# Kernel optimization log

Hardware: AMD Instinct MI355X
Metric: run time of the kernel (lower is better)

## Reference

```python
import jax, jax.numpy as jnp
import numpy as np

N_SEL = 8192      # total nodes across selected subgraphs
SUB_SZ = 32       # nodes per subgraph
N_SUB = 256       # number of subgraphs (N_SEL / SUB_SZ)
N_GRAPH = 64      # source graphs (4 subgraphs each)
N_FULL = 12288    # nodes in the full graph
E_RAW = 262144    # raw edges
N_PERS = 4        # weighted-cosine perspectives
D = 128           # feature dim
EPSILON = 0.1
LAMB1 = 0.5


def setup_inputs() -> dict:
    key = jax.random.key(0)
    k1, k2, k3, k4, k5 = jax.random.split(key, 5)
    x = jax.random.normal(k1, (N_SEL, D), dtype=jnp.float32)
    Wc = jax.random.normal(k2, (N_PERS, D), dtype=jnp.float32)
    selected_score = jax.random.uniform(k3, (N_SUB,), dtype=jnp.float32) + 0.1
    selected_batch = jnp.asarray(np.arange(N_SEL) // SUB_SZ, dtype=jnp.int32)
    selected_belong = jnp.asarray(np.arange(N_SUB) // (N_SUB // N_GRAPH), dtype=jnp.int32)
    # injective mapping from selected nodes -> full-graph node ids
    selected_mapping = jax.random.permutation(k4, N_FULL)[:N_SEL].astype(jnp.int32)
    # block-diagonal complete edge set within each subgraph (torch.meshgrid in prepare_parsed_data)
    base = (np.arange(N_SUB) * SUB_SZ)[:, None, None]
    r = np.broadcast_to(np.arange(SUB_SZ)[None, :, None], (N_SUB, SUB_SZ, SUB_SZ)) + base
    c = np.broadcast_to(np.arange(SUB_SZ)[None, None, :], (N_SUB, SUB_SZ, SUB_SZ)) + base
    full_edge_index = jnp.asarray(np.stack([r.ravel(), c.ravel()]), dtype=jnp.int32)
    raw_edge_index = jax.random.randint(k5, (2, E_RAW), 0, N_FULL, dtype=jnp.int32)
    return {"x": x, "Wc": Wc, "selected_score": selected_score,
            "selected_batch": selected_batch, "selected_mapping": selected_mapping,
            "selected_belong": selected_belong, "full_edge_index": full_edge_index,
            "raw_edge_index": raw_edge_index}


def reference(x, Wc, selected_score, selected_batch, selected_mapping,
              selected_belong, full_edge_index, raw_edge_index):
    # ---- per-graph scatter-normalization of subgraph scores ----
    score_sum = jax.ops.segment_sum(selected_score, selected_belong, num_segments=N_GRAPH)
    score = selected_score / score_sum[selected_belong]          # [N_SUB]

    # ---- WeightedCosine metric: dense pairwise adjacency over all selected nodes ----
    h = x[None, :, :] * Wc[:, None, :]                            # [P, N_sel, D]
    hn = h / jnp.clip(jnp.linalg.norm(h, axis=-1, keepdims=True), 1e-12)
    adj = jnp.einsum('pid,pjd->ij', hn, hn) / N_PERS              # [N_sel, N_sel]

    # ---- mask to intra-subgraph candidate edges ----
    mask = jnp.zeros((N_SEL, N_SEL), dtype=adj.dtype).at[full_edge_index[0], full_edge_index[1]].set(1.0)
    adj = adj * mask
    # EpsilonNN
    adj = adj * (adj > EPSILON).astype(adj.dtype)
    # RemoveSelfLoop
    adj = adj * (1.0 - jnp.eye(N_SEL, dtype=adj.dtype))
    # dense_to_sparse + weighting: weight each edge by its row-node's subgraph score
    attr = adj * (score[selected_batch] * LAMB1)[:, None]         # [N_sel, N_sel]

    # ---- map to full-graph ids and coalesce (duplicate-sum) into dense adjacency ----
    out = jnp.zeros((N_FULL, N_FULL), dtype=x.dtype)
    out = out.at[selected_mapping[:, None], selected_mapping[None, :]].add(attr)
    out = out.at[raw_edge_index[0], raw_edge_index[1]].add(1.0 - LAMB1)
    return out
```

## Files before the change

### kernel.cpp

```cpp
#include <hip/hip_runtime.h>

#define N_SEL 8192
#define SUB_SZ 32
#define N_SUB 256
#define N_GRAPH 64
#define N_FULL 12288
#define E_RAW 262144
#define N_PERS 4
#define D 128
#define EPSILON 0.1f
#define LAMB1 0.5f

#define CAP_E 96
#define OVF_CAP 8192

typedef float f4_t __attribute__((ext_vector_type(4)));

#define OFF_COUNTS   0
#define OFF_INVMAP   ((size_t)N_FULL * 4)
#define OFF_ATTR     (OFF_INVMAP + (size_t)N_FULL * 4)
#define OFF_RAWCOLS  (OFF_ATTR + (size_t)N_SEL * SUB_SZ * 4)
#define OFF_OVFCNT   (OFF_RAWCOLS + (size_t)N_FULL * CAP_E * 4)
#define OFF_OVF      (OFF_OVFCNT + 16)
#define WS_NEEDED    (OFF_OVF + (size_t)OVF_CAP * 8)

__global__ __launch_bounds__(256) void prep_kernel(int* __restrict__ counts,
                                                   int* __restrict__ inv_map,
                                                   int* __restrict__ ovf_cnt)
{
    int t = blockIdx.x * 256 + threadIdx.x;
    if (t < N_FULL) { counts[t] = 0; inv_map[t] = -1; }
    if (t == 0) *ovf_cnt = 0;
}

__global__ __launch_bounds__(256) void build_kernel(
        const float* __restrict__ x,
        const float* __restrict__ Wc,
        const float* __restrict__ sscore,
        const int*   __restrict__ smap,
        const int*   __restrict__ rei,
        int*   __restrict__ counts,
        int*   __restrict__ inv_map,
        float* __restrict__ attr_vals,
        int*   __restrict__ raw_cols,
        int*   __restrict__ ovf_cnt,
        uint2* __restrict__ ovf)
{
    const int tid = threadIdx.x;

    if (blockIdx.x >= N_SUB) {
        int e = (blockIdx.x - N_SUB) * 256 + tid;
        int r = rei[e];
        int c = rei[E_RAW + e];
        int slot = atomicAdd(&counts[r], 1);
        if (slot < CAP_E) {
            raw_cols[(size_t)r * CAP_E + slot] = c;
        } else {
            int o = atomicAdd(ovf_cnt, 1);
            if (o < OVF_CAP) ovf[o] = make_uint2((unsigned)r, (unsigned)c);
        }
        return;
    }

    const int s    = blockIdx.x;
    const int base = s * SUB_SZ;

    __shared__ float xs[SUB_SZ][D + 1];
    __shared__ float w2[N_PERS][D];
    __shared__ float rnorm[N_PERS][SUB_SZ];
    __shared__ float rowscore;

    for (int k = tid; k < SUB_SZ * D; k += 256) {
        int i = k >> 7;
        int d = k & (D - 1);
        xs[i][d] = x[(base + i) * D + d];
    }
    for (int k = tid; k < N_PERS * D; k += 256) {
        float w = Wc[k];
        ((float*)w2)[k] = w * w;
    }
    if (tid < SUB_SZ) inv_map[smap[base + tid]] = base + tid;
    if (tid == 0) {
        int g4 = (s >> 2) << 2;
        float sum = sscore[g4] + sscore[g4 + 1] + sscore[g4 + 2] + sscore[g4 + 3];
        rowscore = (sscore[s] / sum) * LAMB1;
    }
    __syncthreads();

    if (tid < N_PERS * SUB_SZ) {
        int p = tid >> 5;
        int i = tid & 31;
        float acc = 0.f;
        #pragma unroll 8
        for (int d = 0; d < D; ++d) {
            float v = xs[i][d];
            acc = fmaf(v * v, w2[p][d], acc);
        }
        rnorm[p][i] = 1.0f / fmaxf(sqrtf(acc), 1e-12f);
    }
    __syncthreads();

    for (int e = tid; e < SUB_SZ * SUB_SZ; e += 256) {
        int i = e >> 5;
        int j = e & 31;
        float v = 0.f;
        if (i != j) {
            float a0 = 0.f, a1 = 0.f, a2 = 0.f, a3 = 0.f;
            #pragma unroll 8
            for (int d = 0; d < D; ++d) {
                float prod = xs[i][d] * xs[j][d];
                a0 = fmaf(prod, w2[0][d], a0);
                a1 = fmaf(prod, w2[1][d], a1);
                a2 = fmaf(prod, w2[2][d], a2);
                a3 = fmaf(prod, w2[3][d], a3);
            }
            float adj = 0.25f * (a0 * rnorm[0][i] * rnorm[0][j] +
                                 a1 * rnorm[1][i] * rnorm[1][j] +
                                 a2 * rnorm[2][i] * rnorm[2][j] +
                                 a3 * rnorm[3][i] * rnorm[3][j]);
            if (adj > EPSILON) v = adj * rowscore;
        }
        attr_vals[(size_t)base * SUB_SZ + e] = v;
    }
}

__global__ __launch_bounds__(256) void rowfill_kernel(
        const int*   __restrict__ counts,
        const int*   __restrict__ inv_map,
        const float* __restrict__ attr_vals,
        const int*   __restrict__ raw_cols,
        const int*   __restrict__ smap,
        float* __restrict__ out)
{
    __shared__ float row[N_FULL];
    const int r   = blockIdx.x;
    const int tid = threadIdx.x;

    f4_t* row4 = (f4_t*)row;
    const f4_t z = (f4_t){0.f, 0.f, 0.f, 0.f};
    #pragma unroll
    for (int k = 0; k < N_FULL / 4 / 256; ++k)
        row4[tid + k * 256] = z;
    __syncthreads();

    int i = inv_map[r];
    if (i >= 0 && tid < SUB_SZ) {
        float v = attr_vals[(size_t)i * SUB_SZ + tid];
        if (v != 0.f) {
            int c = smap[(i >> 5) * SUB_SZ + tid];
            atomicAdd(&row[c], v);
        }
    }
    int cnt = counts[r];
    if (cnt > CAP_E) cnt = CAP_E;
    for (int e = tid; e < cnt; e += 256) {
        int c = raw_cols[(size_t)r * CAP_E + e];
        atomicAdd(&row[c], 1.0f - LAMB1);
    }
    __syncthreads();

    f4_t* dst = (f4_t*)(out + (size_t)r * N_FULL);
    #pragma unroll
    for (int k = 0; k < N_FULL / 4 / 256; ++k)
        __builtin_nontemporal_store(row4[tid + k * 256], &dst[tid + k * 256]);
}

__global__ __launch_bounds__(256) void ovf_kernel(const int* __restrict__ ovf_cnt,
                                                  const uint2* __restrict__ ovf,
                                                  float* __restrict__ out)
{
    int n = *ovf_cnt;
    if (n > OVF_CAP) n = OVF_CAP;
    for (int t = blockIdx.x * 256 + threadIdx.x; t < n; t += gridDim.x * 256) {
        uint2 e = ovf[t];
        atomicAdd(&out[(size_t)e.x * N_FULL + e.y], 1.0f - LAMB1);
    }
}

#define N4_TOTAL 37748736
#define FILL_BLOCKS 4096
#define PER_BLOCK (N4_TOTAL / FILL_BLOCKS)
#define FILL_ITERS (PER_BLOCK / 256)

__global__ __launch_bounds__(256) void zero_kernel(f4_t* __restrict__ out)
{
    size_t base = (size_t)blockIdx.x * PER_BLOCK + threadIdx.x;
    const f4_t z = (f4_t){0.f, 0.f, 0.f, 0.f};
    #pragma unroll
    for (int k = 0; k < FILL_ITERS; ++k)
        __builtin_nontemporal_store(z, &out[base + (size_t)k * 256]);
}

__global__ __launch_bounds__(256) void scatter_kernel(
        const float* __restrict__ x,
        const float* __restrict__ Wc,
        const float* __restrict__ sscore,
        const int*   __restrict__ smap,
        const int*   __restrict__ rei,
        float* __restrict__ out)
{
    const int tid = threadIdx.x;

    if (blockIdx.x >= N_SUB) {
        int e = (blockIdx.x - N_SUB) * 256 + tid;
        long long r = rei[e];
        long long c = rei[E_RAW + e];
        atomicAdd(&out[r * (long long)N_FULL + c], 1.0f - LAMB1);
        return;
    }

    const int s    = blockIdx.x;
    const int base = s * SUB_SZ;

    __shared__ float xs[SUB_SZ][D + 1];
    __shared__ float w2[N_PERS][D];
    __shared__ float rnorm[N_PERS][SUB_SZ];
    __shared__ int   map_s[SUB_SZ];
    __shared__ float rowscore;

    for (int k = tid; k < SUB_SZ * D; k += 256) {
        int i = k >> 7;
        int d = k & (D - 1);
        xs[i][d] = x[(base + i) * D + d];
    }
    for (int k = tid; k < N_PERS * D; k += 256) {
        float w = Wc[k];
        ((float*)w2)[k] = w * w;
    }
    if (tid < SUB_SZ) map_s[tid] = smap[base + tid];
    if (tid == 0) {
        int g4 = (s >> 2) << 2;
        float sum = sscore[g4] + sscore[g4 + 1] + sscore[g4 + 2] + sscore[g4 + 3];
        rowscore = (sscore[s] / sum) * LAMB1;
    }
    __syncthreads();

    if (tid < N_PERS * SUB_SZ) {
        int p = tid >> 5;
        int i = tid & 31;
        float acc = 0.f;
        #pragma unroll 8
        for (int d = 0; d < D; ++d) {
            float v = xs[i][d];
            acc = fmaf(v * v, w2[p][d], acc);
        }
        rnorm[p][i] = 1.0f / fmaxf(sqrtf(acc), 1e-12f);
    }
    __syncthreads();

    for (int e = tid; e < SUB_SZ * SUB_SZ; e += 256) {
        int i = e >> 5;
        int j = e & 31;
        if (i == j) continue;
        float a0 = 0.f, a1 = 0.f, a2 = 0.f, a3 = 0.f;
        #pragma unroll 8
        for (int d = 0; d < D; ++d) {
            float prod = xs[i][d] * xs[j][d];
            a0 = fmaf(prod, w2[0][d], a0);
            a1 = fmaf(prod, w2[1][d], a1);
            a2 = fmaf(prod, w2[2][d], a2);
            a3 = fmaf(prod, w2[3][d], a3);
        }
        float adj = 0.25f * (a0 * rnorm[0][i] * rnorm[0][j] +
                             a1 * rnorm[1][i] * rnorm[1][j] +
                             a2 * rnorm[2][i] * rnorm[2][j] +
                             a3 * rnorm[3][i] * rnorm[3][j]);
        if (adj > EPSILON) {
            long long row = map_s[i];
            long long col = map_s[j];
            atomicAdd(&out[row * (long long)N_FULL + col], adj * rowscore);
        }
    }
}

extern "C" void kernel_launch(void* const* d_in, const int* in_sizes, int n_in,
                              void* d_out, int out_size, void* d_ws, size_t ws_size,
                              hipStream_t stream) {
    const float* x      = (const float*)d_in[0];
    const float* Wc     = (const float*)d_in[1];
    const float* sscore = (const float*)d_in[2];
    const int* smap = (const int*)d_in[4];
    const int* rei  = (const int*)d_in[7];
    float* out = (float*)d_out;

    if (ws_size >= WS_NEEDED) {
        char* ws = (char*)d_ws;
        int*   counts    = (int*)(ws + OFF_COUNTS);
        int*   inv_map   = (int*)(ws + OFF_INVMAP);
        float* attr_vals = (float*)(ws + OFF_ATTR);
        int*   raw_cols  = (int*)(ws + OFF_RAWCOLS);
        int*   ovf_cnt   = (int*)(ws + OFF_OVFCNT);
        uint2* ovf       = (uint2*)(ws + OFF_OVF);

        prep_kernel<<<(N_FULL + 255) / 256, 256, 0, stream>>>(counts, inv_map, ovf_cnt);
        build_kernel<<<N_SUB + E_RAW / 256, 256, 0, stream>>>(
            x, Wc, sscore, smap, rei, counts, inv_map, attr_vals, raw_cols, ovf_cnt, ovf);
        rowfill_kernel<<<N_FULL, 256, 0, stream>>>(
            counts, inv_map, attr_vals, raw_cols, smap, out);
        ovf_kernel<<<16, 256, 0, stream>>>(ovf_cnt, ovf, out);
    } else {
        zero_kernel<<<FILL_BLOCKS, 256, 0, stream>>>((f4_t*)out);
        scatter_kernel<<<N_SUB + E_RAW / 256, 256, 0, stream>>>(
            x, Wc, sscore, smap, rei, out);
    }
}
```

Measured before the change: 160.4 us.

## Build dense output rows in registers instead of a 48KB shared-memory row

The row-fill kernel no longer zeroes a 48KB shared-memory row and scatters into it with atomics. It stages the up to 128 sparse (column, value) entries for the row in a small shared buffer. Each thread then scans all entries and adds the ones that fall in its own 12 float4 slots, accumulating in registers before streaming the row out. This removes the large LDS footprint that limited occupancy on a store-bandwidth-bound kernel. In exchange every thread does a serial scan of all entries, with a select chain per entry.

```diff
diff --git a/kernel.cpp b/kernel.cpp
--- a/kernel.cpp
+++ b/kernel.cpp
@@ -13,6 +13,7 @@
 
 #define CAP_E 96
 #define OVF_CAP 8192
+#define KROW 12
 
 typedef float f4_t __attribute__((ext_vector_type(4)));
 
@@ -132,37 +133,55 @@
         const int*   __restrict__ smap,
         float* __restrict__ out)
 {
-    __shared__ float row[N_FULL];
+    __shared__ uint2 ents[CAP_E + SUB_SZ];
     const int r   = blockIdx.x;
     const int tid = threadIdx.x;
 
-    f4_t* row4 = (f4_t*)row;
-    const f4_t z = (f4_t){0.f, 0.f, 0.f, 0.f};
-    #pragma unroll
-    for (int k = 0; k < N_FULL / 4 / 256; ++k)
-        row4[tid + k * 256] = z;
-    __syncthreads();
-
-    int i = inv_map[r];
-    if (i >= 0 && tid < SUB_SZ) {
-        float v = attr_vals[(size_t)i * SUB_SZ + tid];
-        if (v != 0.f) {
-            int c = smap[(i >> 5) * SUB_SZ + tid];
-            atomicAdd(&row[c], v);
-        }
-    }
     int cnt = counts[r];
     if (cnt > CAP_E) cnt = CAP_E;
-    for (int e = tid; e < cnt; e += 256) {
-        int c = raw_cols[(size_t)r * CAP_E + e];
-        atomicAdd(&row[c], 1.0f - LAMB1);
-    }
-    __syncthreads();
+    if (tid < cnt)
+        ents[tid] = make_uint2((unsigned)raw_cols[(size_t)r * CAP_E + tid],
+                               __float_as_uint(1.0f - LAMB1));
+    int i = inv_map[r];
+    int n_ent = cnt;
+    if (i >= 0) {
+        if (tid < SUB_SZ) {
+            float v = attr_vals[(size_t)i * SUB_SZ + tid];
+            int   c = smap[(i >> 5) * SUB_SZ + tid];
+            ents[cnt + tid] = make_uint2((unsigned)c, __float_as_uint(v));
+        }
+        n_ent += SUB_SZ;
+    }
+    __syncthreads();
+
+    f4_t acc[KROW];
+    #pragma unroll
+    for (int k = 0; k < KROW; ++k)
+        acc[k] = (f4_t){0.f, 0.f, 0.f, 0.f};
+
+    for (int e = 0; e < n_ent; ++e) {
+        uint2 en = ents[e];
+        unsigned c = en.x;
+        if (((c >> 2) & 255u) == (unsigned)tid) {
+            float v = __uint_as_float(en.y);
+            int k = (int)(c >> 10);
+            int j = (int)(c & 3u);
+            #pragma unroll
+            for (int kk = 0; kk < KROW; ++kk) {
+                if (kk == k) {
+                    acc[kk].x += (j == 0) ? v : 0.f;
+                    acc[kk].y += (j == 1) ? v : 0.f;
+                    acc[kk].z += (j == 2) ? v : 0.f;
+                    acc[kk].w += (j == 3) ? v : 0.f;
+                }
+            }
+        }
+    }
 
     f4_t* dst = (f4_t*)(out + (size_t)r * N_FULL);
     #pragma unroll
-    for (int k = 0; k < N_FULL / 4 / 256; ++k)
-        __builtin_nontemporal_store(row4[tid + k * 256], &dst[tid + k * 256]);
+    for (int k = 0; k < KROW; ++k)
+        __builtin_nontemporal_store(acc[k], &dst[k * 256 + tid]);
 }
 
 __global__ __launch_bounds__(256) void ovf_kernel(const int* __restrict__ ovf_cnt,
```

After: 170.4 us. 6.3% more time.

## Replace per-row LDS assembly with bitmap-guided zero fill plus sparse line patches

Applied to the files above, without the earlier changes.

Builds a bitmap of 64-byte output lines that receive nonzero entries, set by atomics during the build kernel. A single launch then has one set of blocks write zeros only to lines not in the bitmap, while per-row blocks assemble and store only the touched 16-float lines. This removes the per-row 48KB shared-memory zeroing, LDS atomics and full-row copy-out, which limited occupancy. In exchange it adds global atomicOr traffic, a bitmap read for every output vector, and a quadratic leader scan over each row's entries.

```diff
diff --git a/kernel.cpp b/kernel.cpp
--- a/kernel.cpp
+++ b/kernel.cpp
@@ -13,6 +13,8 @@
 
 #define CAP_E 96
 #define OVF_CAP 8192
+#define LPR (N_FULL / 16)
+#define BM_WORDS (N_FULL * LPR / 32)
 
 typedef float f4_t __attribute__((ext_vector_type(4)));
 
@@ -22,13 +24,16 @@
 #define OFF_RAWCOLS  (OFF_ATTR + (size_t)N_SEL * SUB_SZ * 4)
 #define OFF_OVFCNT   (OFF_RAWCOLS + (size_t)N_FULL * CAP_E * 4)
 #define OFF_OVF      (OFF_OVFCNT + 16)
-#define WS_NEEDED    (OFF_OVF + (size_t)OVF_CAP * 8)
+#define OFF_BITMAP   (OFF_OVF + (size_t)OVF_CAP * 8)
+#define WS_NEEDED    (OFF_BITMAP + (size_t)BM_WORDS * 4)
 
 __global__ __launch_bounds__(256) void prep_kernel(int* __restrict__ counts,
                                                    int* __restrict__ inv_map,
-                                                   int* __restrict__ ovf_cnt)
+                                                   int* __restrict__ ovf_cnt,
+                                                   unsigned* __restrict__ bitmap)
 {
     int t = blockIdx.x * 256 + threadIdx.x;
+    if (t < BM_WORDS) bitmap[t] = 0u;
     if (t < N_FULL) { counts[t] = 0; inv_map[t] = -1; }
     if (t == 0) *ovf_cnt = 0;
 }
@@ -44,7 +49,8 @@
         float* __restrict__ attr_vals,
         int*   __restrict__ raw_cols,
         int*   __restrict__ ovf_cnt,
-        uint2* __restrict__ ovf)
+        uint2* __restrict__ ovf,
+        unsigned* __restrict__ bitmap)
 {
     const int tid = threadIdx.x;
 
@@ -55,6 +61,8 @@
         int slot = atomicAdd(&counts[r], 1);
         if (slot < CAP_E) {
             raw_cols[(size_t)r * CAP_E + slot] = c;
+            int line = r * LPR + (c >> 4);
+            atomicOr(&bitmap[line >> 5], 1u << (line & 31));
         } else {
             int o = atomicAdd(ovf_cnt, 1);
             if (o < OVF_CAP) ovf[o] = make_uint2((unsigned)r, (unsigned)c);
@@ -68,6 +76,7 @@
     __shared__ float xs[SUB_SZ][D + 1];
     __shared__ float w2[N_PERS][D];
     __shared__ float rnorm[N_PERS][SUB_SZ];
+    __shared__ int   map_s[SUB_SZ];
     __shared__ float rowscore;
 
     for (int k = tid; k < SUB_SZ * D; k += 256) {
@@ -79,7 +88,11 @@
         float w = Wc[k];
         ((float*)w2)[k] = w * w;
     }
-    if (tid < SUB_SZ) inv_map[smap[base + tid]] = base + tid;
+    if (tid < SUB_SZ) {
+        int m = smap[base + tid];
+        map_s[tid] = m;
+        inv_map[m] = base + tid;
+    }
     if (tid == 0) {
         int g4 = (s >> 2) << 2;
         float sum = sscore[g4] + sscore[g4 + 1] + sscore[g4 + 2] + sscore[g4 + 3];
@@ -118,51 +131,97 @@
                                  a1 * rnorm[1][i] * rnorm[1][j] +
                                  a2 * rnorm[2][i] * rnorm[2][j] +
                                  a3 * rnorm[3][i] * rnorm[3][j]);
-            if (adj > EPSILON) v = adj * rowscore;
+            if (adj > EPSILON) {
+                v = adj * rowscore;
+                int line = map_s[i] * LPR + (map_s[j] >> 4);
+                atomicOr(&bitmap[line >> 5], 1u << (line & 31));
+            }
         }
         attr_vals[(size_t)base * SUB_SZ + e] = v;
     }
 }
 
-__global__ __launch_bounds__(256) void rowfill_kernel(
+#define FILL_BLOCKS 4096
+#define N4_TOTAL 37748736
+#define PER_BLOCK (N4_TOTAL / FILL_BLOCKS)
+#define FILL_ITERS (PER_BLOCK / 256)
+
+__global__ __launch_bounds__(256) void fillpatch_kernel(
         const int*   __restrict__ counts,
         const int*   __restrict__ inv_map,
         const float* __restrict__ attr_vals,
         const int*   __restrict__ raw_cols,
         const int*   __restrict__ smap,
+        const unsigned* __restrict__ bitmap,
         float* __restrict__ out)
 {
-    __shared__ float row[N_FULL];
-    const int r   = blockIdx.x;
     const int tid = threadIdx.x;
 
-    f4_t* row4 = (f4_t*)row;
-    const f4_t z = (f4_t){0.f, 0.f, 0.f, 0.f};
-    #pragma unroll
-    for (int k = 0; k < N_FULL / 4 / 256; ++k)
-        row4[tid + k * 256] = z;
-    __syncthreads();
-
+    if (blockIdx.x >= N_FULL) {
+        const int b = blockIdx.x - N_FULL;
+        const size_t base4 = (size_t)b * PER_BLOCK + tid;
+        const f4_t z = (f4_t){0.f, 0.f, 0.f, 0.f};
+        f4_t* out4 = (f4_t*)out;
+        #pragma unroll
+        for (int k = 0; k < FILL_ITERS; ++k) {
+            size_t idx4 = base4 + (size_t)k * 256;
+            unsigned line = (unsigned)(idx4 >> 2);
+            unsigned w = bitmap[line >> 5];
+            if (!((w >> (line & 31u)) & 1u))
+                __builtin_nontemporal_store(z, &out4[idx4]);
+        }
+        return;
+    }
+
+    const int r = blockIdx.x;
+    __shared__ uint2 ents[CAP_E + SUB_SZ];
+    __shared__ int nloc;
+
+    int cnt = counts[r];
+    if (cnt > CAP_E) cnt = CAP_E;
+    if (tid == 0) nloc = cnt;
+    __syncthreads();
+
+    if (tid < cnt)
+        ents[tid] = make_uint2((unsigned)raw_cols[(size_t)r * CAP_E + tid],
+                               __float_as_uint(1.0f - LAMB1));
     int i = inv_map[r];
     if (i >= 0 && tid < SUB_SZ) {
         float v = attr_vals[(size_t)i * SUB_SZ + tid];
         if (v != 0.f) {
             int c = smap[(i >> 5) * SUB_SZ + tid];
-            atomicAdd(&row[c], v);
-        }
-    }
-    int cnt = counts[r];
-    if (cnt > CAP_E) cnt = CAP_E;
-    for (int e = tid; e < cnt; e += 256) {
-        int c = raw_cols[(size_t)r * CAP_E + e];
-        atomicAdd(&row[c], 1.0f - LAMB1);
-    }
-    __syncthreads();
-
-    f4_t* dst = (f4_t*)(out + (size_t)r * N_FULL);
-    #pragma unroll
-    for (int k = 0; k < N_FULL / 4 / 256; ++k)
-        __builtin_nontemporal_store(row4[tid + k * 256], &dst[tid + k * 256]);
+            int s = atomicAdd(&nloc, 1);
+            ents[s] = make_uint2((unsigned)c, __float_as_uint(v));
+        }
+    }
+    __syncthreads();
+
+    const int n = nloc;
+    for (int e = tid; e < n; e += 256) {
+        unsigned line = ents[e].x >> 4;
+        bool leader = true;
+        for (int e2 = 0; e2 < e; ++e2)
+            if ((ents[e2].x >> 4) == line) { leader = false; break; }
+        if (!leader) continue;
+
+        float vals[16];
+        #pragma unroll
+        for (int q = 0; q < 16; ++q) vals[q] = 0.f;
+        for (int e2 = e; e2 < n; ++e2) {
+            uint2 q2 = ents[e2];
+            if ((q2.x >> 4) == line) {
+                float qv = __uint_as_float(q2.y);
+                int sl = (int)(q2.x & 15u);
+                #pragma unroll
+                for (int q = 0; q < 16; ++q)
+                    vals[q] += (q == sl) ? qv : 0.f;
+            }
+        }
+        f4_t* lp = (f4_t*)(out + (size_t)r * N_FULL + ((size_t)line << 4));
+        #pragma unroll
+        for (int q = 0; q < 4; ++q)
+            __builtin_nontemporal_store(((f4_t*)vals)[q], &lp[q]);
+    }
 }
 
 __global__ __launch_bounds__(256) void ovf_kernel(const int* __restrict__ ovf_cnt,
@@ -176,11 +235,6 @@
         atomicAdd(&out[(size_t)e.x * N_FULL + e.y], 1.0f - LAMB1);
     }
 }
-
-#define N4_TOTAL 37748736
-#define FILL_BLOCKS 4096
-#define PER_BLOCK (N4_TOTAL / FILL_BLOCKS)
-#define FILL_ITERS (PER_BLOCK / 256)
 
 __global__ __launch_bounds__(256) void zero_kernel(f4_t* __restrict__ out)
 {
@@ -285,18 +339,20 @@
 
     if (ws_size >= WS_NEEDED) {
         char* ws = (char*)d_ws;
-        int*   counts    = (int*)(ws + OFF_COUNTS);
-        int*   inv_map   = (int*)(ws + OFF_INVMAP);
-        float* attr_vals = (float*)(ws + OFF_ATTR);
-        int*   raw_cols  = (int*)(ws + OFF_RAWCOLS);
-        int*   ovf_cnt   = (int*)(ws + OFF_OVFCNT);
-        uint2* ovf       = (uint2*)(ws + OFF_OVF);
-
-        prep_kernel<<<(N_FULL + 255) / 256, 256, 0, stream>>>(counts, inv_map, ovf_cnt);
+        int*      counts    = (int*)(ws + OFF_COUNTS);
+        int*      inv_map   = (int*)(ws + OFF_INVMAP);
+        float*    attr_vals = (float*)(ws + OFF_ATTR);
+        int*      raw_cols  = (int*)(ws + OFF_RAWCOLS);
+        int*      ovf_cnt   = (int*)(ws + OFF_OVFCNT);
+        uint2*    ovf       = (uint2*)(ws + OFF_OVF);
+        unsigned* bitmap    = (unsigned*)(ws + OFF_BITMAP);
+
+        prep_kernel<<<BM_WORDS / 256, 256, 0, stream>>>(counts, inv_map, ovf_cnt, bitmap);
         build_kernel<<<N_SUB + E_RAW / 256, 256, 0, stream>>>(
-            x, Wc, sscore, smap, rei, counts, inv_map, attr_vals, raw_cols, ovf_cnt, ovf);
-        rowfill_kernel<<<N_FULL, 256, 0, stream>>>(
-            counts, inv_map, attr_vals, raw_cols, smap, out);
+            x, Wc, sscore, smap, rei, counts, inv_map, attr_vals, raw_cols,
+            ovf_cnt, ovf, bitmap);
+        fillpatch_kernel<<<N_FULL + FILL_BLOCKS, 256, 0, stream>>>(
+            counts, inv_map, attr_vals, raw_cols, smap, bitmap, out);
         ovf_kernel<<<16, 256, 0, stream>>>(ovf_cnt, ovf, out);
     } else {
         zero_kernel<<<FILL_BLOCKS, 256, 0, stream>>>((f4_t*)out);
```

New measurement: 198.2 us. 23.5% more time.

## Fuse prep, build, rowfill and overflow into one cooperative grid-synced kernel

Applied to the files above, without the earlier changes.

Replaces four kernel launches with a single cooperative kernel of 1024 blocks that uses grid-wide syncs between phases: init, raw-edge bucketing plus subgraph cosine, row fill, overflow. Row fill no longer builds each 48KB row in shared memory. It writes zeros straight to global memory and then applies the few edge values with global atomics, gathering them in a small shared list first. This is meant to cut launch overhead and the large LDS footprint that limited occupancy. The costs are grid-sync overhead, only 4 blocks per CU with each block handling 12 rows serially, and global atomics racing against the block's own zero stores, which are ordered only by __syncthreads.

```diff
diff --git a/kernel.cpp b/kernel.cpp
--- a/kernel.cpp
+++ b/kernel.cpp
@@ -1,4 +1,7 @@
 #include <hip/hip_runtime.h>
+#include <hip/hip_cooperative_groups.h>
+
+namespace cg = cooperative_groups;
 
 #define N_SEL 8192
 #define SUB_SZ 32
@@ -13,6 +16,9 @@
 
 #define CAP_E 96
 #define OVF_CAP 8192
+#define GRID_B 1024
+#define ROWS_PER_B (N_FULL / GRID_B)
+#define COS_BASE (GRID_B - N_SUB)
 
 typedef float f4_t __attribute__((ext_vector_type(4)));
 
@@ -24,16 +30,7 @@
 #define OFF_OVF      (OFF_OVFCNT + 16)
 #define WS_NEEDED    (OFF_OVF + (size_t)OVF_CAP * 8)
 
-__global__ __launch_bounds__(256) void prep_kernel(int* __restrict__ counts,
-                                                   int* __restrict__ inv_map,
-                                                   int* __restrict__ ovf_cnt)
-{
-    int t = blockIdx.x * 256 + threadIdx.x;
-    if (t < N_FULL) { counts[t] = 0; inv_map[t] = -1; }
-    if (t == 0) *ovf_cnt = 0;
-}
-
-__global__ __launch_bounds__(256) void build_kernel(
+__global__ __launch_bounds__(256, 4) void fused_kernel(
         const float* __restrict__ x,
         const float* __restrict__ Wc,
         const float* __restrict__ sscore,
@@ -44,12 +41,30 @@
         float* __restrict__ attr_vals,
         int*   __restrict__ raw_cols,
         int*   __restrict__ ovf_cnt,
-        uint2* __restrict__ ovf)
+        uint2* __restrict__ ovf,
+        float* __restrict__ out)
 {
+    cg::grid_group grid = cg::this_grid();
     const int tid = threadIdx.x;
-
-    if (blockIdx.x >= N_SUB) {
-        int e = (blockIdx.x - N_SUB) * 256 + tid;
+    const int b   = blockIdx.x;
+
+    __shared__ float xs[SUB_SZ][D + 1];
+    __shared__ float w2v[N_PERS][D];
+    __shared__ float rnorm[N_PERS][SUB_SZ];
+    __shared__ float rowscore;
+    __shared__ unsigned ecol[CAP_E + SUB_SZ];
+    __shared__ float    evalv[CAP_E + SUB_SZ];
+    __shared__ int nloc;
+
+    for (int t = b * 256 + tid; t < N_FULL; t += GRID_B * 256) {
+        counts[t]  = 0;
+        inv_map[t] = -1;
+    }
+    if (b == 0 && tid == 0) *ovf_cnt = 0;
+    grid.sync();
+
+    {
+        int e = b * 256 + tid;
         int r = rei[e];
         int c = rei[E_RAW + e];
         int slot = atomicAdd(&counts[r], 1);
@@ -59,119 +74,105 @@
             int o = atomicAdd(ovf_cnt, 1);
             if (o < OVF_CAP) ovf[o] = make_uint2((unsigned)r, (unsigned)c);
         }
-        return;
-    }
-
-    const int s    = blockIdx.x;
-    const int base = s * SUB_SZ;
-
-    __shared__ float xs[SUB_SZ][D + 1];
-    __shared__ float w2[N_PERS][D];
-    __shared__ float rnorm[N_PERS][SUB_SZ];
-    __shared__ float rowscore;
-
-    for (int k = tid; k < SUB_SZ * D; k += 256) {
-        int i = k >> 7;
-        int d = k & (D - 1);
-        xs[i][d] = x[(base + i) * D + d];
-    }
-    for (int k = tid; k < N_PERS * D; k += 256) {
-        float w = Wc[k];
-        ((float*)w2)[k] = w * w;
-    }
-    if (tid < SUB_SZ) inv_map[smap[base + tid]] = base + tid;
-    if (tid == 0) {
-        int g4 = (s >> 2) << 2;
-        float sum = sscore[g4] + sscore[g4 + 1] + sscore[g4 + 2] + sscore[g4 + 3];
-        rowscore = (sscore[s] / sum) * LAMB1;
-    }
-    __syncthreads();
-
-    if (tid < N_PERS * SUB_SZ) {
-        int p = tid >> 5;
-        int i = tid & 31;
-        float acc = 0.f;
-        #pragma unroll 8
-        for (int d = 0; d < D; ++d) {
-            float v = xs[i][d];
-            acc = fmaf(v * v, w2[p][d], acc);
-        }
-        rnorm[p][i] = 1.0f / fmaxf(sqrtf(acc), 1e-12f);
-    }
-    __syncthreads();
-
-    for (int e = tid; e < SUB_SZ * SUB_SZ; e += 256) {
-        int i = e >> 5;
-        int j = e & 31;
-        float v = 0.f;
-        if (i != j) {
-            float a0 = 0.f, a1 = 0.f, a2 = 0.f, a3 = 0.f;
+    }
+    if (b >= COS_BASE) {
+        const int s    = b - COS_BASE;
+        const int base = s * SUB_SZ;
+
+        for (int k = tid; k < SUB_SZ * D; k += 256) {
+            int i = k >> 7;
+            int d = k & (D - 1);
+            xs[i][d] = x[(base + i) * D + d];
+        }
+        for (int k = tid; k < N_PERS * D; k += 256) {
+            float w = Wc[k];
+            ((float*)w2v)[k] = w * w;
+        }
+        if (tid < SUB_SZ) inv_map[smap[base + tid]] = base + tid;
+        if (tid == 0) {
+            int g4 = (s >> 2) << 2;
+            float sum = sscore[g4] + sscore[g4 + 1] + sscore[g4 + 2] + sscore[g4 + 3];
+            rowscore = (sscore[s] / sum) * LAMB1;
+        }
+        __syncthreads();
+
+        if (tid < N_PERS * SUB_SZ) {
+            int p = tid >> 5;
+            int i = tid & 31;
+            float acc = 0.f;
             #pragma unroll 8
             for (int d = 0; d < D; ++d) {
-                float prod = xs[i][d] * xs[j][d];
-                a0 = fmaf(prod, w2[0][d], a0);
-                a1 = fmaf(prod, w2[1][d], a1);
-                a2 = fmaf(prod, w2[2][d], a2);
-                a3 = fmaf(prod, w2[3][d], a3);
+                float v = xs[i][d];
+                acc = fmaf(v * v, w2v[p][d], acc);
             }
-            float adj = 0.25f * (a0 * rnorm[0][i] * rnorm[0][j] +
-                                 a1 * rnorm[1][i] * rnorm[1][j] +
-                                 a2 * rnorm[2][i] * rnorm[2][j] +
-                                 a3 * rnorm[3][i] * rnorm[3][j]);
-            if (adj > EPSILON) v = adj * rowscore;
-        }
-        attr_vals[(size_t)base * SUB_SZ + e] = v;
-    }
-}
-
-__global__ __launch_bounds__(256) void rowfill_kernel(
-        const int*   __restrict__ counts,
-        const int*   __restrict__ inv_map,
-        const float* __restrict__ attr_vals,
-        const int*   __restrict__ raw_cols,
-        const int*   __restrict__ smap,
-        float* __restrict__ out)
-{
-    __shared__ float row[N_FULL];
-    const int r   = blockIdx.x;
-    const int tid = threadIdx.x;
-
-    f4_t* row4 = (f4_t*)row;
+            rnorm[p][i] = 1.0f / fmaxf(sqrtf(acc), 1e-12f);
+        }
+        __syncthreads();
+
+        for (int e = tid; e < SUB_SZ * SUB_SZ; e += 256) {
+            int i = e >> 5;
+            int j = e & 31;
+            float v = 0.f;
+            if (i != j) {
+                float a0 = 0.f, a1 = 0.f, a2 = 0.f, a3 = 0.f;
+                #pragma unroll 8
+                for (int d = 0; d < D; ++d) {
+                    float prod = xs[i][d] * xs[j][d];
+                    a0 = fmaf(prod, w2v[0][d], a0);
+                    a1 = fmaf(prod, w2v[1][d], a1);
+                    a2 = fmaf(prod, w2v[2][d], a2);
+                    a3 = fmaf(prod, w2v[3][d], a3);
+                }
+                float adj = 0.25f * (a0 * rnorm[0][i] * rnorm[0][j] +
+                                     a1 * rnorm[1][i] * rnorm[1][j] +
+                                     a2 * rnorm[2][i] * rnorm[2][j] +
+                                     a3 * rnorm[3][i] * rnorm[3][j]);
+                if (adj > EPSILON) v = adj * rowscore;
+            }
+            attr_vals[(size_t)base * SUB_SZ + e] = v;
+        }
+    }
+    grid.sync();
+
     const f4_t z = (f4_t){0.f, 0.f, 0.f, 0.f};
-    #pragma unroll
-    for (int k = 0; k < N_FULL / 4 / 256; ++k)
-        row4[tid + k * 256] = z;
-    __syncthreads();
-
-    int i = inv_map[r];
-    if (i >= 0 && tid < SUB_SZ) {
-        float v = attr_vals[(size_t)i * SUB_SZ + tid];
-        if (v != 0.f) {
-            int c = smap[(i >> 5) * SUB_SZ + tid];
-            atomicAdd(&row[c], v);
-        }
-    }
-    int cnt = counts[r];
-    if (cnt > CAP_E) cnt = CAP_E;
-    for (int e = tid; e < cnt; e += 256) {
-        int c = raw_cols[(size_t)r * CAP_E + e];
-        atomicAdd(&row[c], 1.0f - LAMB1);
-    }
-    __syncthreads();
-
-    f4_t* dst = (f4_t*)(out + (size_t)r * N_FULL);
-    #pragma unroll
-    for (int k = 0; k < N_FULL / 4 / 256; ++k)
-        __builtin_nontemporal_store(row4[tid + k * 256], &dst[tid + k * 256]);
-}
-
-__global__ __launch_bounds__(256) void ovf_kernel(const int* __restrict__ ovf_cnt,
-                                                  const uint2* __restrict__ ovf,
-                                                  float* __restrict__ out)
-{
+    for (int r = b * ROWS_PER_B; r < (b + 1) * ROWS_PER_B; ++r) {
+        int cnt = counts[r];
+        if (cnt > CAP_E) cnt = CAP_E;
+        if (tid == 0) nloc = cnt;
+        __syncthreads();
+
+        if (tid < cnt) {
+            ecol[tid]  = (unsigned)raw_cols[(size_t)r * CAP_E + tid];
+            evalv[tid] = 1.0f - LAMB1;
+        }
+        int i = inv_map[r];
+        if (i >= 0 && tid < SUB_SZ) {
+            float v = attr_vals[(size_t)i * SUB_SZ + tid];
+            if (v != 0.f) {
+                int s2 = atomicAdd(&nloc, 1);
+                ecol[s2]  = (unsigned)smap[(i >> 5) * SUB_SZ + tid];
+                evalv[s2] = v;
+            }
+        }
+
+        f4_t* dst = (f4_t*)(out + (size_t)r * N_FULL);
+        #pragma unroll
+        for (int k = 0; k < N_FULL / 4 / 256; ++k)
+            dst[k * 256 + tid] = z;
+
+        __syncthreads();
+
+        int n = nloc;
+        float* base = out + (size_t)r * N_FULL;
+        for (int e = tid; e < n; e += 256)
+            atomicAdd(&base[ecol[e]], evalv[e]);
+        __syncthreads();
+    }
+    grid.sync();
+
     int n = *ovf_cnt;
     if (n > OVF_CAP) n = OVF_CAP;
-    for (int t = blockIdx.x * 256 + threadIdx.x; t < n; t += gridDim.x * 256) {
+    for (int t = b * 256 + tid; t < n; t += GRID_B * 256) {
         uint2 e = ovf[t];
         atomicAdd(&out[(size_t)e.x * N_FULL + e.y], 1.0f - LAMB1);
     }
@@ -283,6 +284,7 @@
     const int* rei  = (const int*)d_in[7];
     float* out = (float*)d_out;
 
+    bool coop_ok = false;
     if (ws_size >= WS_NEEDED) {
         char* ws = (char*)d_ws;
         int*   counts    = (int*)(ws + OFF_COUNTS);
@@ -292,13 +294,17 @@
         int*   ovf_cnt   = (int*)(ws + OFF_OVFCNT);
         uint2* ovf       = (uint2*)(ws + OFF_OVF);
 
-        prep_kernel<<<(N_FULL + 255) / 256, 256, 0, stream>>>(counts, inv_map, ovf_cnt);
-        build_kernel<<<N_SUB + E_RAW / 256, 256, 0, stream>>>(
-            x, Wc, sscore, smap, rei, counts, inv_map, attr_vals, raw_cols, ovf_cnt, ovf);
-        rowfill_kernel<<<N_FULL, 256, 0, stream>>>(
-            counts, inv_map, attr_vals, raw_cols, smap, out);
-        ovf_kernel<<<16, 256, 0, stream>>>(ovf_cnt, ovf, out);
-    } else {
+        void* args[] = {
+            (void*)&x, (void*)&Wc, (void*)&sscore, (void*)&smap, (void*)&rei,
+            (void*)&counts, (void*)&inv_map, (void*)&attr_vals, (void*)&raw_cols,
+            (void*)&ovf_cnt, (void*)&ovf, (void*)&out
+        };
+        hipError_t err = hipLaunchCooperativeKernel(
+            (void*)fused_kernel, dim3(GRID_B), dim3(256), args, 0, stream);
+        coop_ok = (err == hipSuccess);
+    }
+
+    if (!coop_ok) {
         zero_kernel<<<FILL_BLOCKS, 256, 0, stream>>>((f4_t*)out);
         scatter_kernel<<<N_SUB + E_RAW / 256, 256, 0, stream>>>(
             x, Wc, sscore, smap, rei, out);
```

Result: slower. 515.3 us (+221.3%).
